# Kernel optimization log

Hardware: AMD Instinct MI355X
Metric: run time of the kernel (lower is better)

Reference implementation:

```python
import jax, jax.numpy as jnp
import numpy as np

NEG_SLOPE = 0.2  # PyG GATConv default negative_slope


def gat_conv(x, src, dst, W, a_src, a_dst, b, concat):
    # x: [N, F_in]; src/dst: [E] edge endpoints (edge j->i means src=j, dst=i)
    N = x.shape[0]
    H, C = a_src.shape
    xp = (x @ W).reshape(N, H, C)                      # per-head projection
    al_s = jnp.einsum('nhc,hc->nh', xp, a_src)          # source attention logits
    al_d = jnp.einsum('nhc,hc->nh', xp, a_dst)          # destination attention logits
    e = jax.nn.leaky_relu(al_s[src] + al_d[dst], NEG_SLOPE)   # [E, H]
    # segment softmax over incoming edges of each destination node
    m = jax.ops.segment_max(e, dst, num_segments=N)     # [N, H]
    m = jnp.where(jnp.isfinite(m), m, jnp.zeros_like(m))
    ex = jnp.exp(e - m[dst])
    den = jax.ops.segment_sum(ex, dst, num_segments=N)  # [N, H]
    alpha = ex / (den[dst] + 1e-16)                     # [E, H]
    out = jax.ops.segment_sum(xp[src] * alpha[:, :, None], dst, num_segments=N)  # [N,H,C]
    out = out.reshape(N, H * C) if concat else out.mean(axis=1)
    return out + b


def setup_inputs() -> dict:
    key = jax.random.key(0)
    ks = jax.random.split(key, 9)
    N, E, F_in, H, C = 50000, 1600000, 128, 4, 32
    x = jax.random.normal(ks[0], (N, F_in), dtype=jnp.float32)
    edge_index = jax.random.randint(ks[1], (2, E), 0, N, dtype=jnp.int64)
    s1 = 1.0 / np.sqrt(F_in)
    s2 = 1.0 / np.sqrt(H * C)
    return {
        'x': x,
        'edge_index': edge_index,
        'W1': jax.random.normal(ks[2], (F_in, H * C), dtype=jnp.float32) * s1,
        'a_src1': jax.random.normal(ks[3], (H, C), dtype=jnp.float32) * s1,
        'a_dst1': jax.random.normal(ks[4], (H, C), dtype=jnp.float32) * s1,
        'b1': jnp.zeros((H * C,), dtype=jnp.float32),
        'W2': jax.random.normal(ks[5], (H * C, C), dtype=jnp.float32) * s2,
        'a_src2': jax.random.normal(ks[6], (1, C), dtype=jnp.float32) * s2,
        'a_dst2': jax.random.normal(ks[7], (1, C), dtype=jnp.float32) * s2,
        'b2': jnp.zeros((C,), dtype=jnp.float32),
    }


def reference(x, edge_index, W1, a_src1, a_dst1, b1, W2, a_src2, a_dst2, b2):
    N = x.shape[0]
    loops = jnp.arange(N, dtype=edge_index.dtype)
    src = jnp.concatenate([edge_index[0], loops])   # PyG default add_self_loops=True
    dst = jnp.concatenate([edge_index[1], loops])
    h = gat_conv(x, src, dst, W1, a_src1, a_dst1, b1, concat=True)
    h = jax.nn.elu(h)
    out = gat_conv(h, src, dst, W2, a_src2, a_dst2, b2, concat=False)
    return out
```

## Files before the change

kernel.cpp:

```cpp
#include <hip/hip_runtime.h>
#include <hip/hip_fp16.h>

#define NEG_SLOPE 0.2f
#define CAP 128
#define NB  64
#define GAB 192

typedef __half half_t;

__device__ __forceinline__ float lrelu(float x) { return x >= 0.f ? x : NEG_SLOPE * x; }

__device__ __forceinline__ unsigned int f2h2(float a, float b) {
    union { unsigned int u; __half2 h; } v; v.h = __floats2half2_rn(a, b);
    return v.u;
}

__device__ __forceinline__ void fma8h(const uint4& v, float w, float* a) {
    const __half* hp = (const __half*)&v;
    #pragma unroll
    for (int j = 0; j < 8; ++j) a[j] = fmaf(w, __half2float(hp[j]), a[j]);
}

__device__ __forceinline__ bool edge_is64(const int* __restrict__ ei, int E) {
    int t = threadIdx.x & 63;
    int idx = 2 * t + 1; if (idx >= 2 * E) idx = 2 * E - 1;
    unsigned long long b = __ballot(ei[idx] != 0);
    return b == 0ULL;
}

__device__ __forceinline__ void load_edge(const int* __restrict__ ei, int E, int i,
                                          bool is64, int& s, int& d) {
    if (i < E) {
        if (is64) { const long long* e = (const long long*)ei; s = (int)e[i]; d = (int)e[E + i]; }
        else      { s = ei[i]; d = ei[E + i]; }
    } else { s = d = i - E; }
}

__global__ __launch_bounds__(256) void k_count(const int* __restrict__ ei,
        int E, int N, int shift, int* __restrict__ partials) {
    __shared__ int cnts[NB];
    int t = threadIdx.x, b = blockIdx.x;
    if (t < NB) cnts[t] = 0;
    bool is64 = edge_is64(ei, E);
    __syncthreads();
    int tot = E + N;
    for (int i = b * 256 + t; i < tot; i += GAB * 256) {
        int s, d; load_edge(ei, E, i, is64, s, d);
        atomicAdd(&cnts[d >> shift], 1);
    }
    __syncthreads();
    if (t < NB) partials[b * NB + t] = cnts[t];
}

__global__ __launch_bounds__(256) void k_scan(int* __restrict__ partials,
                                              int* __restrict__ bin_base) {
    __shared__ int lp[GAB * NB];
    __shared__ int tot[NB], base[NB];
    int t = threadIdx.x;
    for (int i = t; i < GAB * NB; i += 256) lp[i] = partials[i];
    __syncthreads();
    if (t < NB) {
        int run = 0;
        for (int b = 0; b < GAB; ++b) { int v = lp[b * NB + t]; lp[b * NB + t] = run; run += v; }
        tot[t] = run;
    }
    __syncthreads();
    if (t == 0) {
        int run = 0;
        for (int i = 0; i < NB; ++i) { base[i] = run; run += tot[i]; }
    }
    __syncthreads();
    if (t < NB) bin_base[t] = base[t];
    if (t == 0) bin_base[NB] = base[NB - 1] + tot[NB - 1];
    for (int i = t; i < GAB * NB; i += 256) partials[i] = lp[i] + base[i & (NB - 1)];
}

__global__ __launch_bounds__(256) void k_bin(const int* __restrict__ ei,
        int E, int N, int shift, const int* __restrict__ offsets, int2* __restrict__ binned) {
    __shared__ int cur[NB];
    int t = threadIdx.x, b = blockIdx.x;
    if (t < NB) cur[t] = offsets[b * NB + t];
    bool is64 = edge_is64(ei, E);
    __syncthreads();
    int tot = E + N;
    for (int i = b * 256 + t; i < tot; i += GAB * 256) {
        int s, d; load_edge(ei, E, i, is64, s, d);
        int pos = atomicAdd(&cur[d >> shift], 1);
        binned[pos] = make_int2(s, d);
    }
}

__global__ __launch_bounds__(1024) void k_part(const int2* __restrict__ binned,
        const int* __restrict__ bin_base, int* __restrict__ off, int* __restrict__ csr,
        int N, int shift) {
    __shared__ int cnt_loc[1024];
    __shared__ int scan_loc[1024];
    __shared__ int wsum[16];
    int b = blockIdx.x, t = threadIdx.x;
    int base = b << shift;
    int span = 1 << shift;
    int lo = bin_base[b], hi = bin_base[b + 1];
    if (t < span) cnt_loc[t] = 0;
    __syncthreads();
    for (int i = lo + t; i < hi; i += 1024)
        atomicAdd(&cnt_loc[binned[i].y - base], 1);
    __syncthreads();
    int v = (t < span) ? cnt_loc[t] : 0;
    int lane = t & 63, w = t >> 6;
    int incl = v;
    #pragma unroll
    for (int m = 1; m < 64; m <<= 1) {
        int u = __shfl_up(incl, m);
        if (lane >= m) incl += u;
    }
    if (lane == 63) wsum[w] = incl;
    __syncthreads();
    if (t == 0) {
        int run = 0;
        #pragma unroll
        for (int i2 = 0; i2 < 16; ++i2) { int s2 = wsum[i2]; wsum[i2] = run; run += s2; }
    }
    __syncthreads();
    int excl = incl - v + wsum[w];
    if (t < span) { scan_loc[t] = lo + excl; off[base + t] = lo + excl; }
    __syncthreads();
    if (t < span) cnt_loc[t] = 0;
    __syncthreads();
    for (int i = lo + t; i < hi; i += 1024) {
        int2 e = binned[i];
        int r = e.y - base;
        int pos = scan_loc[r] + atomicAdd(&cnt_loc[r], 1);
        csr[pos] = e.x;
    }
}

__global__ __launch_bounds__(256) void gemm1_kernel(const float* __restrict__ x,
        const float* __restrict__ W1, const float* __restrict__ a_src,
        const float* __restrict__ a_dst, half_t* __restrict__ xp1h,
        float* __restrict__ al_s, float* __restrict__ al_d, int N) {
    __shared__ __align__(16) float xst[64 * 128];
    __shared__ __align__(16) float ws[64 * 128];
    int t = threadIdx.x;
    int row0 = blockIdx.x * 128;
    int cg = t & 15, rg = t >> 4;
    float acc[8][8] = {};
    for (int chunk = 0; chunk < 2; ++chunk) {
        __syncthreads();
        int c0 = chunk * 64;
        #pragma unroll
        for (int ii = 0; ii < 8; ++ii) {
            int idx = t + 256 * ii;
            int r = idx >> 4, kq = idx & 15;
            int n = row0 + r;
            float4 v = make_float4(0.f, 0.f, 0.f, 0.f);
            if (n < N) v = *(const float4*)&x[(size_t)n * 128 + c0 + kq * 4];
            float vv[4] = {v.x, v.y, v.z, v.w};
            #pragma unroll
            for (int j = 0; j < 4; ++j) {
                int k = kq * 4 + j;
                xst[k * 128 + (((r >> 2) ^ (k & 31)) << 2) + (r & 3)] = vv[j];
            }
        }
        #pragma unroll
        for (int ii = 0; ii < 8; ++ii) {
            int idx = t + 256 * ii;
            int k = idx >> 5, cq = idx & 31;
            *(float4*)&ws[k * 128 + cq * 4] =
                *(const float4*)&W1[(size_t)(c0 + k) * 128 + cq * 4];
        }
        __syncthreads();
        int g0 = rg * 2, g1 = rg * 2 + 1;
        #pragma unroll 4
        for (int k = 0; k < 64; ++k) {
            int kb = k & 31;
            float4 xv0 = *(const float4*)&xst[k * 128 + ((g0 ^ kb) << 2)];
            float4 xv1 = *(const float4*)&xst[k * 128 + ((g1 ^ kb) << 2)];
            float4 wv0 = *(const float4*)&ws[k * 128 + cg * 8];
            float4 wv1 = *(const float4*)&ws[k * 128 + cg * 8 + 4];
            float xr[8] = {xv0.x, xv0.y, xv0.z, xv0.w, xv1.x, xv1.y, xv1.z, xv1.w};
            float wr[8] = {wv0.x, wv0.y, wv0.z, wv0.w, wv1.x, wv1.y, wv1.z, wv1.w};
            #pragma unroll
            for (int r = 0; r < 8; ++r)
                #pragma unroll
                for (int c = 0; c < 8; ++c)
                    acc[r][c] = fmaf(xr[r], wr[c], acc[r][c]);
        }
    }
    #pragma unroll
    for (int r = 0; r < 8; ++r) {
        int n = row0 + rg * 8 + r;
        if (n < N) {
            uint4 u = make_uint4(f2h2(acc[r][0], acc[r][1]), f2h2(acc[r][2], acc[r][3]),
                                 f2h2(acc[r][4], acc[r][5]), f2h2(acc[r][6], acc[r][7]));
            *(uint4*)&xp1h[(size_t)n * 128 + cg * 8] = u;
        }
    }
    float ps[8], pd[8];
    #pragma unroll
    for (int r = 0; r < 8; ++r) {
        float s = 0.f, dd = 0.f;
        #pragma unroll
        for (int c = 0; c < 8; ++c) {
            s  = fmaf(acc[r][c], a_src[cg * 8 + c], s);
            dd = fmaf(acc[r][c], a_dst[cg * 8 + c], dd);
        }
        ps[r] = s; pd[r] = dd;
    }
    #pragma unroll
    for (int m = 1; m < 4; m <<= 1) {
        #pragma unroll
        for (int r = 0; r < 8; ++r) { ps[r] += __shfl_xor(ps[r], m); pd[r] += __shfl_xor(pd[r], m); }
    }
    if ((cg & 3) == 0) {
        int head = cg >> 2;
        #pragma unroll
        for (int r = 0; r < 8; ++r) {
            int n = row0 + rg * 8 + r;
            if (n < N) { al_s[n * 4 + head] = ps[r]; al_d[n * 4 + head] = pd[r]; }
        }
    }
}

__global__ __launch_bounds__(128) void edge1_kernel(const int* __restrict__ off,
        const int* __restrict__ csr, const float* __restrict__ al_s,
        const float* __restrict__ al_d, const half_t* __restrict__ xp1h,
        const float* __restrict__ b1, half_t* __restrict__ h1h, int N) {
    __shared__ int srcs[CAP];
    __shared__ float ew[CAP * 4];
    __shared__ __align__(16) float red[8 * 128];
    __shared__ float4 wden[2];
    __shared__ float rinv_s[4];
    int d = blockIdx.x, t = threadIdx.x;
    int o0 = off[d], o1 = off[d + 1];
    int deg = o1 - o0; if (deg > CAP) deg = CAP;
    float4 ex = make_float4(0.f, 0.f, 0.f, 0.f);
    if (t < deg) {
        int s = csr[o0 + t];
        srcs[t] = s;
        float4 as = *(const float4*)&al_s[s * 4];
        float4 ad = *(const float4*)&al_d[d * 4];
        ex.x = __expf(lrelu(as.x + ad.x));
        ex.y = __expf(lrelu(as.y + ad.y));
        ex.z = __expf(lrelu(as.z + ad.z));
        ex.w = __expf(lrelu(as.w + ad.w));
        *(float4*)&ew[t * 4] = ex;
    }
    float4 r = ex;
    #pragma unroll
    for (int m = 1; m < 64; m <<= 1) {
        r.x += __shfl_xor(r.x, m); r.y += __shfl_xor(r.y, m);
        r.z += __shfl_xor(r.z, m); r.w += __shfl_xor(r.w, m);
    }
    if ((t & 63) == 0) wden[t >> 6] = r;
    __syncthreads();
    float4 den = wden[0], dn1 = wden[1];
    den.x += dn1.x; den.y += dn1.y; den.z += dn1.z; den.w += dn1.w;
    if (t < 4)
        rinv_s[t] = 1.f / ((t == 0 ? den.x : t == 1 ? den.y : t == 2 ? den.z : den.w) + 1e-16f);
    int q = t & 15, p = t >> 4, h = q >> 2;
    float a[8] = {};
    const uint4* xr = (const uint4*)xp1h;
    for (int i = p; i < deg; i += 8) {
        float wv = ew[i * 4 + h];
        uint4 v = xr[(size_t)srcs[i] * 16 + q];
        fma8h(v, wv, a);
    }
    *(float4*)&red[p * 128 + q * 8 + 0] = make_float4(a[0], a[1], a[2], a[3]);
    *(float4*)&red[p * 128 + q * 8 + 4] = make_float4(a[4], a[5], a[6], a[7]);
    __syncthreads();
    float sum = 0.f;
    #pragma unroll
    for (int pp = 0; pp < 8; ++pp) sum += red[pp * 128 + t];
    float v = sum * rinv_s[t >> 5] + b1[t];
    h1h[(size_t)d * 128 + t] = __float2half(v > 0.f ? v : expm1f(v));
}

__global__ __launch_bounds__(256) void gemm2l_kernel(const half_t* __restrict__ h1h,
        const float* __restrict__ W2, const float* __restrict__ a_s2,
        const float* __restrict__ a_d2, half_t* __restrict__ xp2h,
        float* __restrict__ al_s2, float* __restrict__ al_d2, int N) {
    __shared__ __align__(16) float w2s[128 * 32];
    int t = threadIdx.x;
    #pragma unroll
    for (int ii = 0; ii < 4; ++ii)
        ((float4*)w2s)[t + 256 * ii] = ((const float4*)W2)[t + 256 * ii];
    if (blockIdx.x == 0 && t < 2)
        ((uint4*)(xp2h + (size_t)N * 32))[t] = make_uint4(0, 0, 0, 0);
    __syncthreads();
    int n = blockIdx.x * 64 + (t >> 2), sub = t & 3;
    if (n >= N) return;
    const uint4* hr = (const uint4*)(h1h + (size_t)n * 128);
    float acc[8] = {};
    #pragma unroll 2
    for (int kq = 0; kq < 16; ++kq) {
        uint4 hv = hr[kq];
        const __half* hp = (const __half*)&hv;
        #pragma unroll
        for (int jj = 0; jj < 8; ++jj) {
            float h = __half2float(hp[jj]);
            int k = kq * 8 + jj;
            float4 wa = *(const float4*)&w2s[k * 32 + sub * 8];
            float4 wb = *(const float4*)&w2s[k * 32 + sub * 8 + 4];
            acc[0] = fmaf(h, wa.x, acc[0]); acc[1] = fmaf(h, wa.y, acc[1]);
            acc[2] = fmaf(h, wa.z, acc[2]); acc[3] = fmaf(h, wa.w, acc[3]);
            acc[4] = fmaf(h, wb.x, acc[4]); acc[5] = fmaf(h, wb.y, acc[5]);
            acc[6] = fmaf(h, wb.z, acc[6]); acc[7] = fmaf(h, wb.w, acc[7]);
        }
    }
    uint4 u = make_uint4(f2h2(acc[0], acc[1]), f2h2(acc[2], acc[3]),
                         f2h2(acc[4], acc[5]), f2h2(acc[6], acc[7]));
    *(uint4*)&xp2h[(size_t)n * 32 + sub * 8] = u;
    float ps = 0.f, pd = 0.f;
    #pragma unroll
    for (int c = 0; c < 8; ++c) {
        ps = fmaf(acc[c], a_s2[sub * 8 + c], ps);
        pd = fmaf(acc[c], a_d2[sub * 8 + c], pd);
    }
    ps += __shfl_xor(ps, 1); ps += __shfl_xor(ps, 2);
    pd += __shfl_xor(pd, 1); pd += __shfl_xor(pd, 2);
    if (sub == 0) { al_s2[n] = ps; al_d2[n] = pd; }
}

__global__ __launch_bounds__(128) void edge2_kernel(const int* __restrict__ off,
        const int* __restrict__ csr, const float* __restrict__ al_s,
        const float* __restrict__ al_d, const half_t* __restrict__ xp2h,
        const float* __restrict__ b2v, float* __restrict__ out, int N) {
    __shared__ int srcs[CAP];
    __shared__ float ew[CAP];
    __shared__ __align__(16) float red[32 * 32];
    __shared__ float red2[128];
    __shared__ float wden[2];
    int d = blockIdx.x, t = threadIdx.x;
    int o0 = off[d], o1 = off[d + 1];
    int deg = o1 - o0; if (deg > CAP) deg = CAP;
    float ex = 0.f;
    int s = N;
    if (t < deg) {
        s = csr[o0 + t];
        ex = __expf(lrelu(al_s[s] + al_d[d]));
    }
    srcs[t] = s;
    float r = ex;
    #pragma unroll
    for (int m = 1; m < 64; m <<= 1) r += __shfl_xor(r, m);
    if ((t & 63) == 0) wden[t >> 6] = r;
    __syncthreads();
    float rinv = 1.f / (wden[0] + wden[1] + 1e-16f);
    ew[t] = ex * rinv;
    __syncthreads();
    int q = t & 3, p = t >> 2;
    float a[8] = {};
    const uint4* xr = (const uint4*)xp2h;
    if (deg <= 32) {
        uint4 v0 = xr[(size_t)srcs[p] * 4 + q];
        fma8h(v0, ew[p], a);
    } else {
        int degp = (deg + 63) & ~63;
        for (int rr = 0; rr < degp; rr += 64) {
            int i0 = rr + p, i1 = i0 + 32;
            uint4 v0 = xr[(size_t)srcs[i0] * 4 + q];
            uint4 v1 = xr[(size_t)srcs[i1] * 4 + q];
            float w0 = ew[i0], w1 = ew[i1];
            fma8h(v0, w0, a); fma8h(v1, w1, a);
        }
    }
    *(float4*)&red[p * 32 + q * 8 + 0] = make_float4(a[0], a[1], a[2], a[3]);
    *(float4*)&red[p * 32 + q * 8 + 4] = make_float4(a[4], a[5], a[6], a[7]);
    __syncthreads();
    int c = t & 31, g = t >> 5;
    float part = 0.f;
    #pragma unroll
    for (int k = 0; k < 8; ++k) part += red[(g * 8 + k) * 32 + c];
    red2[t] = part;
    __syncthreads();
    if (t < 32) {
        float s2 = red2[t] + red2[t + 32] + red2[t + 64] + red2[t + 96];
        out[(size_t)d * 32 + t] = s2 + b2v[t];
    }
}

extern "C" void kernel_launch(void* const* d_in, const int* in_sizes, int n_in,
                              void* d_out, int out_size, void* d_ws, size_t ws_size,
                              hipStream_t stream) {
    const float* x    = (const float*)d_in[0];
    const int*   ei   = (const int*)d_in[1];
    const float* W1   = (const float*)d_in[2];
    const float* a_s1 = (const float*)d_in[3];
    const float* a_d1 = (const float*)d_in[4];
    const float* b1   = (const float*)d_in[5];
    const float* W2   = (const float*)d_in[6];
    const float* a_s2 = (const float*)d_in[7];
    const float* a_d2 = (const float*)d_in[8];
    const float* b2   = (const float*)d_in[9];
    int N = in_sizes[0] / 128;
    int E = in_sizes[1] / 2;
    float* out = (float*)d_out;

    int shift = 0;
    while (((N - 1) >> shift) >= NB) shift++;

    char* wsb = (char*)d_ws;
    size_t off_b = 0;
    auto alloc = [&](size_t bytes) -> void* {
        void* p = wsb + off_b;
        off_b = (off_b + bytes + 255) & ~(size_t)255;
        return p;
    };
    int*    partials = (int*)   alloc((size_t)GAB * NB * 4);
    int*    bin_base = (int*)   alloc((size_t)(NB + 1) * 4);
    int2*   binned   = (int2*)  alloc((size_t)(E + N) * 8);
    int*    offs     = (int*)   alloc(((size_t)NB << shift) * 4 + 8);
    int*    csr      = (int*)   alloc((size_t)(E + N) * 4);
    half_t* xp1h     = (half_t*)alloc((size_t)(N + 1) * 128 * 2);
    float*  al_s1    = (float*) alloc((size_t)N * 4 * 4);
    float*  al_d1    = (float*) alloc((size_t)N * 4 * 4);
    half_t* h1h      = (half_t*)alloc((size_t)N * 128 * 2);
    half_t* xp2h     = (half_t*)alloc((size_t)(N + 1) * 32 * 2);
    float*  al_s2    = (float*) alloc((size_t)N * 4);
    float*  al_d2    = (float*) alloc((size_t)N * 4);

    k_count<<<GAB, 256, 0, stream>>>(ei, E, N, shift, partials);
    k_scan<<<1, 256, 0, stream>>>(partials, bin_base);
    k_bin<<<GAB, 256, 0, stream>>>(ei, E, N, shift, partials, binned);
    k_part<<<NB, 1024, 0, stream>>>(binned, bin_base, offs, csr, N, shift);
    gemm1_kernel<<<(N + 127) / 128, 256, 0, stream>>>(x, W1, a_s1, a_d1, xp1h, al_s1, al_d1, N);
    edge1_kernel<<<N, 128, 0, stream>>>(offs, csr, al_s1, al_d1, xp1h, b1, h1h, N);
    gemm2l_kernel<<<(N + 63) / 64, 256, 0, stream>>>(h1h, W2, a_s2, a_d2, xp2h, al_s2, al_d2, N);
    edge2_kernel<<<N, 128, 0, stream>>>(offs, csr, al_s2, al_d2, xp2h, b2, out, N);
}
```

Before: 297.2 us.

## Map one wavefront per destination node in GAT edge kernels

Both edge aggregation kernels now give each destination node a single 64-lane wavefront, with four nodes per 256-thread block, instead of a whole 128-thread block per node. Block-level shared-memory reductions and __syncthreads are replaced by wavefront shuffles, and the output is written as vectorized half/float stores. The intent is to remove block sync and LDS reduction overhead and to cut launch granularity for low-degree nodes. In exchange each wavefront covers more edges serially, which lowers the number of gather loads in flight per node. Shared-memory reads of ew and srcs written by other lanes now rely on wavefront lockstep rather than an explicit barrier.

```diff
diff --git a/kernel.cpp b/kernel.cpp
--- a/kernel.cpp
+++ b/kernel.cpp
@@ -221,58 +221,82 @@
     }
 }
 
-__global__ __launch_bounds__(128) void edge1_kernel(const int* __restrict__ off,
+__global__ __launch_bounds__(256) void edge1_kernel(const int* __restrict__ off,
         const int* __restrict__ csr, const float* __restrict__ al_s,
         const float* __restrict__ al_d, const half_t* __restrict__ xp1h,
         const float* __restrict__ b1, half_t* __restrict__ h1h, int N) {
-    __shared__ int srcs[CAP];
-    __shared__ float ew[CAP * 4];
-    __shared__ __align__(16) float red[8 * 128];
-    __shared__ float4 wden[2];
-    __shared__ float rinv_s[4];
-    int d = blockIdx.x, t = threadIdx.x;
+    __shared__ int   srcs[4][CAP];
+    __shared__ float ew[4][CAP * 4];
+    int t = threadIdx.x;
+    int wid = t >> 6, lane = t & 63;
+    int d = blockIdx.x * 4 + wid;
+    if (d >= N) return;
     int o0 = off[d], o1 = off[d + 1];
     int deg = o1 - o0; if (deg > CAP) deg = CAP;
-    float4 ex = make_float4(0.f, 0.f, 0.f, 0.f);
-    if (t < deg) {
-        int s = csr[o0 + t];
-        srcs[t] = s;
+    float4 ad = *(const float4*)&al_d[d * 4];
+    float4 ex0 = make_float4(0.f, 0.f, 0.f, 0.f);
+    float4 ex1 = make_float4(0.f, 0.f, 0.f, 0.f);
+    if (lane < deg) {
+        int s = csr[o0 + lane];
+        srcs[wid][lane] = s;
         float4 as = *(const float4*)&al_s[s * 4];
-        float4 ad = *(const float4*)&al_d[d * 4];
-        ex.x = __expf(lrelu(as.x + ad.x));
-        ex.y = __expf(lrelu(as.y + ad.y));
-        ex.z = __expf(lrelu(as.z + ad.z));
-        ex.w = __expf(lrelu(as.w + ad.w));
-        *(float4*)&ew[t * 4] = ex;
-    }
-    float4 r = ex;
+        ex0.x = __expf(lrelu(as.x + ad.x));
+        ex0.y = __expf(lrelu(as.y + ad.y));
+        ex0.z = __expf(lrelu(as.z + ad.z));
+        ex0.w = __expf(lrelu(as.w + ad.w));
+    }
+    if (lane + 64 < deg) {
+        int s = csr[o0 + lane + 64];
+        srcs[wid][lane + 64] = s;
+        float4 as = *(const float4*)&al_s[s * 4];
+        ex1.x = __expf(lrelu(as.x + ad.x));
+        ex1.y = __expf(lrelu(as.y + ad.y));
+        ex1.z = __expf(lrelu(as.z + ad.z));
+        ex1.w = __expf(lrelu(as.w + ad.w));
+    }
+    float4 r = make_float4(ex0.x + ex1.x, ex0.y + ex1.y, ex0.z + ex1.z, ex0.w + ex1.w);
     #pragma unroll
     for (int m = 1; m < 64; m <<= 1) {
         r.x += __shfl_xor(r.x, m); r.y += __shfl_xor(r.y, m);
         r.z += __shfl_xor(r.z, m); r.w += __shfl_xor(r.w, m);
     }
-    if ((t & 63) == 0) wden[t >> 6] = r;
-    __syncthreads();
-    float4 den = wden[0], dn1 = wden[1];
-    den.x += dn1.x; den.y += dn1.y; den.z += dn1.z; den.w += dn1.w;
-    if (t < 4)
-        rinv_s[t] = 1.f / ((t == 0 ? den.x : t == 1 ? den.y : t == 2 ? den.z : den.w) + 1e-16f);
-    int q = t & 15, p = t >> 4, h = q >> 2;
+    float4 ri = make_float4(1.f / (r.x + 1e-16f), 1.f / (r.y + 1e-16f),
+                            1.f / (r.z + 1e-16f), 1.f / (r.w + 1e-16f));
+    if (lane < deg)
+        *(float4*)&ew[wid][lane * 4] =
+            make_float4(ex0.x * ri.x, ex0.y * ri.y, ex0.z * ri.z, ex0.w * ri.w);
+    if (lane + 64 < deg)
+        *(float4*)&ew[wid][(lane + 64) * 4] =
+            make_float4(ex1.x * ri.x, ex1.y * ri.y, ex1.z * ri.z, ex1.w * ri.w);
+    int q = lane & 15, p = lane >> 4, h = q >> 2;
     float a[8] = {};
     const uint4* xr = (const uint4*)xp1h;
-    for (int i = p; i < deg; i += 8) {
-        float wv = ew[i * 4 + h];
-        uint4 v = xr[(size_t)srcs[i] * 16 + q];
-        fma8h(v, wv, a);
-    }
-    *(float4*)&red[p * 128 + q * 8 + 0] = make_float4(a[0], a[1], a[2], a[3]);
-    *(float4*)&red[p * 128 + q * 8 + 4] = make_float4(a[4], a[5], a[6], a[7]);
-    __syncthreads();
-    float sum = 0.f;
-    #pragma unroll
-    for (int pp = 0; pp < 8; ++pp) sum += red[pp * 128 + t];
-    float v = sum * rinv_s[t >> 5] + b1[t];
-    h1h[(size_t)d * 128 + t] = __float2half(v > 0.f ? v : expm1f(v));
+    for (int i = p; i < deg; i += 4) {
+        float w = ew[wid][i * 4 + h];
+        uint4 v = xr[(size_t)srcs[wid][i] * 16 + q];
+        fma8h(v, w, a);
+    }
+    #pragma unroll
+    for (int j = 0; j < 8; ++j) {
+        a[j] += __shfl_xor(a[j], 16);
+        a[j] += __shfl_xor(a[j], 32);
+    }
+    if (p == 0) {
+        float4 b0 = *(const float4*)&b1[q * 8];
+        float4 b4 = *(const float4*)&b1[q * 8 + 4];
+        float v0 = a[0] + b0.x, v1 = a[1] + b0.y, v2 = a[2] + b0.z, v3 = a[3] + b0.w;
+        float v4 = a[4] + b4.x, v5 = a[5] + b4.y, v6 = a[6] + b4.z, v7 = a[7] + b4.w;
+        v0 = v0 > 0.f ? v0 : expm1f(v0);
+        v1 = v1 > 0.f ? v1 : expm1f(v1);
+        v2 = v2 > 0.f ? v2 : expm1f(v2);
+        v3 = v3 > 0.f ? v3 : expm1f(v3);
+        v4 = v4 > 0.f ? v4 : expm1f(v4);
+        v5 = v5 > 0.f ? v5 : expm1f(v5);
+        v6 = v6 > 0.f ? v6 : expm1f(v6);
+        v7 = v7 > 0.f ? v7 : expm1f(v7);
+        uint4 u = make_uint4(f2h2(v0, v1), f2h2(v2, v3), f2h2(v4, v5), f2h2(v6, v7));
+        *(uint4*)&h1h[(size_t)d * 128 + q * 8] = u;
+    }
 }
 
 __global__ __launch_bounds__(256) void gemm2l_kernel(const half_t* __restrict__ h1h,
@@ -321,61 +345,58 @@
     if (sub == 0) { al_s2[n] = ps; al_d2[n] = pd; }
 }
 
-__global__ __launch_bounds__(128) void edge2_kernel(const int* __restrict__ off,
+__global__ __launch_bounds__(256) void edge2_kernel(const int* __restrict__ off,
         const int* __restrict__ csr, const float* __restrict__ al_s,
         const float* __restrict__ al_d, const half_t* __restrict__ xp2h,
         const float* __restrict__ b2v, float* __restrict__ out, int N) {
-    __shared__ int srcs[CAP];
-    __shared__ float ew[CAP];
-    __shared__ __align__(16) float red[32 * 32];
-    __shared__ float red2[128];
-    __shared__ float wden[2];
-    int d = blockIdx.x, t = threadIdx.x;
+    __shared__ int   srcs[4][CAP];
+    __shared__ float ew[4][CAP];
+    int t = threadIdx.x;
+    int wid = t >> 6, lane = t & 63;
+    int d = blockIdx.x * 4 + wid;
+    if (d >= N) return;
     int o0 = off[d], o1 = off[d + 1];
     int deg = o1 - o0; if (deg > CAP) deg = CAP;
-    float ex = 0.f;
-    int s = N;
-    if (t < deg) {
-        s = csr[o0 + t];
-        ex = __expf(lrelu(al_s[s] + al_d[d]));
-    }
-    srcs[t] = s;
-    float r = ex;
+    float adv = al_d[d];
+    float ex0 = 0.f, ex1 = 0.f;
+    if (lane < deg) {
+        int s = csr[o0 + lane];
+        srcs[wid][lane] = s;
+        ex0 = __expf(lrelu(al_s[s] + adv));
+    }
+    if (lane + 64 < deg) {
+        int s = csr[o0 + lane + 64];
+        srcs[wid][lane + 64] = s;
+        ex1 = __expf(lrelu(al_s[s] + adv));
+    }
+    float r = ex0 + ex1;
     #pragma unroll
     for (int m = 1; m < 64; m <<= 1) r += __shfl_xor(r, m);
-    if ((t & 63) == 0) wden[t >> 6] = r;
-    __syncthreads();
-    float rinv = 1.f / (wden[0] + wden[1] + 1e-16f);
-    ew[t] = ex * rinv;
-    __syncthreads();
-    int q = t & 3, p = t >> 2;
+    float rinv = 1.f / (r + 1e-16f);
+    if (lane < deg)      ew[wid][lane]      = ex0 * rinv;
+    if (lane + 64 < deg) ew[wid][lane + 64] = ex1 * rinv;
+    int q = lane & 3, p = lane >> 2;
     float a[8] = {};
     const uint4* xr = (const uint4*)xp2h;
-    if (deg <= 32) {
-        uint4 v0 = xr[(size_t)srcs[p] * 4 + q];
-        fma8h(v0, ew[p], a);
-    } else {
-        int degp = (deg + 63) & ~63;
-        for (int rr = 0; rr < degp; rr += 64) {
-            int i0 = rr + p, i1 = i0 + 32;
-            uint4 v0 = xr[(size_t)srcs[i0] * 4 + q];
-            uint4 v1 = xr[(size_t)srcs[i1] * 4 + q];
-            float w0 = ew[i0], w1 = ew[i1];
-            fma8h(v0, w0, a); fma8h(v1, w1, a);
-        }
-    }
-    *(float4*)&red[p * 32 + q * 8 + 0] = make_float4(a[0], a[1], a[2], a[3]);
-    *(float4*)&red[p * 32 + q * 8 + 4] = make_float4(a[4], a[5], a[6], a[7]);
-    __syncthreads();
-    int c = t & 31, g = t >> 5;
-    float part = 0.f;
-    #pragma unroll
-    for (int k = 0; k < 8; ++k) part += red[(g * 8 + k) * 32 + c];
-    red2[t] = part;
-    __syncthreads();
-    if (t < 32) {
-        float s2 = red2[t] + red2[t + 32] + red2[t + 64] + red2[t + 96];
-        out[(size_t)d * 32 + t] = s2 + b2v[t];
+    for (int i = p; i < deg; i += 16) {
+        float w = ew[wid][i];
+        uint4 v = xr[(size_t)srcs[wid][i] * 4 + q];
+        fma8h(v, w, a);
+    }
+    #pragma unroll
+    for (int j = 0; j < 8; ++j) {
+        a[j] += __shfl_xor(a[j], 4);
+        a[j] += __shfl_xor(a[j], 8);
+        a[j] += __shfl_xor(a[j], 16);
+        a[j] += __shfl_xor(a[j], 32);
+    }
+    if (p == 0) {
+        float4 b0 = *(const float4*)&b2v[q * 8];
+        float4 b4 = *(const float4*)&b2v[q * 8 + 4];
+        float4 o0v = make_float4(a[0] + b0.x, a[1] + b0.y, a[2] + b0.z, a[3] + b0.w);
+        float4 o1v = make_float4(a[4] + b4.x, a[5] + b4.y, a[6] + b4.z, a[7] + b4.w);
+        *(float4*)&out[(size_t)d * 32 + q * 8]     = o0v;
+        *(float4*)&out[(size_t)d * 32 + q * 8 + 4] = o1v;
     }
 }
 
@@ -424,7 +445,7 @@
     k_bin<<<GAB, 256, 0, stream>>>(ei, E, N, shift, partials, binned);
     k_part<<<NB, 1024, 0, stream>>>(binned, bin_base, offs, csr, N, shift);
     gemm1_kernel<<<(N + 127) / 128, 256, 0, stream>>>(x, W1, a_s1, a_d1, xp1h, al_s1, al_d1, N);
-    edge1_kernel<<<N, 128, 0, stream>>>(offs, csr, al_s1, al_d1, xp1h, b1, h1h, N);
+    edge1_kernel<<<(N + 3) / 4, 256, 0, stream>>>(offs, csr, al_s1, al_d1, xp1h, b1, h1h, N);
     gemm2l_kernel<<<(N + 63) / 64, 256, 0, stream>>>(h1h, W2, a_s2, a_d2, xp2h, al_s2, al_d2, N);
-    edge2_kernel<<<N, 128, 0, stream>>>(offs, csr, al_s2, al_d2, xp2h, b2, out, N);
-}
+    edge2_kernel<<<(N + 3) / 4, 256, 0, stream>>>(offs, csr, al_s2, al_d2, xp2h, b2, out, N);
+}
```

New measurement: 290.2 us. 2.4% less time.
